# Kernel optimization log

Hardware: AMD Instinct MI355X
Metric: run time of the kernel (lower is better)

## Reference

```python
import jax, jax.numpy as jnp
import numpy as np

B, T, D_IN, H, K, C = 8, 2048, 512, 384, 8192, 8
N_BLOCKS = 6
EPS = 1e-5


def conv1d(x, w, b, pad, groups=1):
    # x: [B, Cin, T], w: [Cout, Cin//groups, k]
    y = jax.lax.conv_general_dilated(
        x, w, window_strides=(1,), padding=[(pad, pad)],
        dimension_numbers=("NCH", "OIH", "NCH"), feature_group_count=groups)
    return y + b[None, :, None]


def layernorm(x, g, b):
    # normalize over last axis
    m = jnp.mean(x, axis=-1, keepdims=True)
    v = jnp.mean(jnp.square(x - m), axis=-1, keepdims=True)
    return (x - m) * jax.lax.rsqrt(v + EPS) * g + b


def setup_inputs() -> dict:
    key = jax.random.key(0)
    ks = iter(jax.random.split(key, 32))
    s = 0.02
    inp = {
        "x": jax.random.normal(next(ks), (B, T, D_IN), dtype=jnp.float32),
        "enc_w": jax.random.normal(next(ks), (H, D_IN, 7)) * s,
        "enc_b": jnp.zeros((H,)),
        "enc_ln_g": jnp.ones((H,)),
        "enc_ln_b": jnp.zeros((H,)),
        "blk_dw_w": jax.random.normal(next(ks), (N_BLOCKS, H, 1, 7)) * s,
        "blk_dw_b": jnp.zeros((N_BLOCKS, H)),
        "blk_ln_g": jnp.ones((N_BLOCKS, H)),
        "blk_ln_b": jnp.zeros((N_BLOCKS, H)),
        "blk_w1": jax.random.normal(next(ks), (N_BLOCKS, 4 * H, H)) * s,
        "blk_b1": jnp.zeros((N_BLOCKS, 4 * H)),
        "blk_w2": jax.random.normal(next(ks), (N_BLOCKS, H, 4 * H)) * s,
        "blk_b2": jnp.zeros((N_BLOCKS, H)),
        "out_w": jax.random.normal(next(ks), (C, H, 1)) * s,
        "out_b": jnp.zeros((C,)),
        "embeddings": jax.random.normal(next(ks), (K, C)),
    }
    return inp


def encode(x, enc_w, enc_b, enc_ln_g, enc_ln_b, blk_dw_w, blk_dw_b,
           blk_ln_g, blk_ln_b, blk_w1, blk_b1, blk_w2, blk_b2, out_w, out_b):
    h = x.transpose(0, 2, 1)                       # [B, D_IN, T]
    h = conv1d(h, enc_w, enc_b, pad=3)             # [B, H, T]
    h = layernorm(h.transpose(0, 2, 1), enc_ln_g, enc_ln_b).transpose(0, 2, 1)
    for i in range(N_BLOCKS):
        res = h
        h = conv1d(h, blk_dw_w[i], blk_dw_b[i], pad=3, groups=H)  # depthwise
        ht = h.transpose(0, 2, 1)                  # [B, T, H]
        ht = layernorm(ht, blk_ln_g[i], blk_ln_b[i])
        ht = jnp.einsum("bth,fh->btf", ht, blk_w1[i]) + blk_b1[i]
        ht = jax.nn.gelu(ht, approximate=False)    # torch GELU is exact erf
        ht = jnp.einsum("btf,hf->bth", ht, blk_w2[i]) + blk_b2[i]
        h = ht.transpose(0, 2, 1) + res
    z = conv1d(h, out_w, out_b, pad=0)             # [B, C, T]
    return z.transpose(0, 2, 1)                    # [B, T, C]


def reference(x, enc_w, enc_b, enc_ln_g, enc_ln_b, blk_dw_w, blk_dw_b,
              blk_ln_g, blk_ln_b, blk_w1, blk_b1, blk_w2, blk_b2,
              out_w, out_b, embeddings):
    z = encode(x, enc_w, enc_b, enc_ln_g, enc_ln_b, blk_dw_w, blk_dw_b,
               blk_ln_g, blk_ln_b, blk_w1, blk_b1, blk_w2, blk_b2, out_w, out_b)
    flat = z.reshape(-1, C)                        # [B*T, C]
    # squared euclidean distances: same argmin as torch.cdist
    d2 = (jnp.sum(flat * flat, axis=1, keepdims=True)
          - 2.0 * flat @ embeddings.T
          + jnp.sum(embeddings * embeddings, axis=1))  # [B*T, K]
    indices = jnp.argmin(d2, axis=1)               # [B*T], int
    return indices
```

## Files before the change

### kernel.cpp

```cpp
#include <hip/hip_runtime.h>
#include <math.h>

#define T_   2048
#define DIN  512
#define H_   384
#define H4_  1536
#define BT_  16384

typedef _Float16 half_t;
typedef _Float16 f16x8 __attribute__((ext_vector_type(8)));
typedef float f32x4 __attribute__((ext_vector_type(4)));

#define LO_SCALE 2048.0f
#define LO_INV   4.8828125e-4f

__device__ __forceinline__ void lds_barrier() {
    asm volatile("s_waitcnt lgkmcnt(0)\n\ts_barrier" ::: "memory");
}

__device__ __forceinline__ void vm_barrier() {
    asm volatile("s_waitcnt vmcnt(0) lgkmcnt(0)\n\ts_barrier" ::: "memory");
}

__device__ __forceinline__ void gload_lds(const half_t* g, half_t* l) {
    __builtin_amdgcn_global_load_lds(
        (const __attribute__((address_space(1))) unsigned int*)(const void*)g,
        (__attribute__((address_space(3))) unsigned int*)(void*)l, 16, 0, 0);
}

__device__ __forceinline__ void split2(float v, half_t* hi, half_t* lo) {
    half_t h = (half_t)v;
    *hi = h;
    *lo = (half_t)((v - (float)h) * LO_SCALE);
}

__global__ void k_split(const float* __restrict__ in, half_t* __restrict__ hi,
                        half_t* __restrict__ lo, long n) {
    long i = (long)blockIdx.x * 256 + threadIdx.x;
    if (i >= n) return;
    split2(in[i], hi + i, lo + i);
}

__global__ void k_split_encw(const float* __restrict__ in, half_t* __restrict__ hi,
                             half_t* __restrict__ lo) {
    int idx = blockIdx.x * 256 + threadIdx.x;
    if (idx >= H_ * 3584) return;
    int n = idx / 3584;
    int r = idx % 3584;
    int tap = r >> 9, i = r & 511;
    split2(in[n * 3584 + i * 7 + tap], hi + idx, lo + idx);
}

__global__ void k_ln(const float* __restrict__ in, float* __restrict__ out,
                     const float* __restrict__ g, const float* __restrict__ b) {
    int row = blockIdx.x;
    int lane = threadIdx.x;
    const float* ir = in + (long)row * H_;
    float v[6];
    float s = 0.f;
#pragma unroll
    for (int j = 0; j < 6; ++j) { v[j] = ir[lane + (j << 6)]; s += v[j]; }
#pragma unroll
    for (int o = 32; o > 0; o >>= 1) s += __shfl_down(s, o, 64);
    s = __shfl(s, 0, 64);
    float mean = s * (1.f / 384.f);
    float q = 0.f;
#pragma unroll
    for (int j = 0; j < 6; ++j) { float d = v[j] - mean; q += d * d; }
#pragma unroll
    for (int o = 32; o > 0; o >>= 1) q += __shfl_down(q, o, 64);
    q = __shfl(q, 0, 64);
    float rstd = rsqrtf(q * (1.f / 384.f) + 1e-5f);
    float* orow = out + (long)row * H_;
#pragma unroll
    for (int j = 0; j < 6; ++j) {
        int c = lane + (j << 6);
        orow[c] = (v[j] - mean) * rstd * g[c] + b[c];
    }
}

__global__ __launch_bounds__(256) void k_dwconv_ln(
    const float* __restrict__ h, half_t* __restrict__ oh,
    half_t* __restrict__ ol,
    const float* __restrict__ w, const float* __restrict__ wb,
    const float* __restrict__ g, const float* __restrict__ gb) {
    int row = (blockIdx.x << 2) + (threadIdx.x >> 6);
    int b = row >> 11;
    int t = row & 2047;
    int lane = threadIdx.x & 63;
    const float* hb = h + ((long)b * T_) * H_;
    float vx[3], vy[3];
    float s = 0.f;
#pragma unroll
    for (int j = 0; j < 3; ++j) {
        int c = (lane << 1) + (j << 7);
        float ax = wb[c], ay = wb[c + 1];
        const float* wcx = w + c * 7;
        const float* wcy = wcx + 7;
#pragma unroll
        for (int k = 0; k < 7; ++k) {
            int tt = t + k - 3;
            if ((unsigned)tt < (unsigned)T_) {
                float2 hv = *(const float2*)&hb[(long)tt * H_ + c];
                ax = fmaf(hv.x, wcx[k], ax);
                ay = fmaf(hv.y, wcy[k], ay);
            }
        }
        vx[j] = ax; vy[j] = ay;
        s += ax + ay;
    }
#pragma unroll
    for (int o = 32; o > 0; o >>= 1) s += __shfl_down(s, o, 64);
    s = __shfl(s, 0, 64);
    float mean = s * (1.f / 384.f);
    float q = 0.f;
#pragma unroll
    for (int j = 0; j < 3; ++j) {
        float dx = vx[j] - mean, dy = vy[j] - mean;
        q += dx * dx + dy * dy;
    }
#pragma unroll
    for (int o = 32; o > 0; o >>= 1) q += __shfl_down(q, o, 64);
    q = __shfl(q, 0, 64);
    float rstd = rsqrtf(q * (1.f / 384.f) + 1e-5f);
    long ro = (long)row * H_;
#pragma unroll
    for (int j = 0; j < 3; ++j) {
        int c = (lane << 1) + (j << 7);
        float valx = (vx[j] - mean) * rstd * g[c] + gb[c];
        float valy = (vy[j] - mean) * rstd * g[c + 1] + gb[c + 1];
        split2(valx, oh + ro + c, ol + ro + c);
        split2(valy, oh + ro + c + 1, ol + ro + c + 1);
    }
}

#define DECLSET(S) float4 pAh##S, pAl##S, pBh0##S, pBl0##S, pBh1##S, pBl1##S

#define LOADREGS(S, k0_) do {                                               \
    int k0v = (k0_);                                                        \
    if (MODE == 0) {                                                        \
        int kk = k0v + ak;                                                  \
        int tap = kk >> 9, ii = kk & 511;                                   \
        int ta = tt0 + tap;                                                 \
        pAh##S = pAl##S = make_float4(0.f, 0.f, 0.f, 0.f);                  \
        if ((unsigned)ta < 2048u) {                                         \
            long o = ((long)bq * 2048 + ta) * 512 + ii;                     \
            pAh##S = *(const float4*)(Ah + o);                              \
            pAl##S = *(const float4*)(Al + o);                              \
        }                                                                   \
    } else {                                                                \
        pAh##S = *(const float4*)(Ah + aoff + k0v);                         \
        pAl##S = *(const float4*)(Al + aoff + k0v);                         \
    }                                                                       \
    pBh0##S = *(const float4*)(Bh + boff0 + k0v);                           \
    pBl0##S = *(const float4*)(Bl + boff0 + k0v);                           \
    pBh1##S = *(const float4*)(Bh + boff1 + k0v);                           \
    pBl1##S = *(const float4*)(Bl + boff1 + k0v);                           \
} while (0)

#define STOREBUF(S, buf) do {                                               \
    *(float4*)&smem[(buf) * 2048 + aw] = pAh##S;                            \
    *(float4*)&smem[4096 + (buf) * 2048 + aw] = pAl##S;                     \
    int b_ = 8192 + (buf) * 4096 + aw;                                      \
    *(float4*)&smem[b_] = pBh0##S;                                          \
    *(float4*)&smem[b_ + 2048] = pBh1##S;                                   \
    *(float4*)&smem[b_ + 8192] = pBl0##S;                                   \
    *(float4*)&smem[b_ + 8192 + 2048] = pBl1##S;                            \
} while (0)

template <int MODE, int NN>
__global__ __launch_bounds__(256, 3) void k_mgemm64(
    const half_t* __restrict__ Ah, const half_t* __restrict__ Al,
    const half_t* __restrict__ Bh, const half_t* __restrict__ Bl,
    const float* __restrict__ bias, const float* __restrict__ res,
    float* __restrict__ Cf, half_t* __restrict__ Ch, half_t* __restrict__ Cl,
    int N, int K) {
    __shared__ __align__(16) half_t smem[24576];
    const int tid = threadIdx.x;
    const int lane = tid & 63, wid = tid >> 6;
    const int wn = wid << 5;
    const int quad = lane >> 4, l16 = lane & 15;

    constexpr int NWG = 256 * NN;
    constexpr int CHUNK = NWG / 8;
    const int lin = blockIdx.x;
    const int tile = (lin & 7) * CHUNK + (lin >> 3);
    const int m0 = (tile / NN) << 6;
    const int n0 = (tile % NN) << 7;

    const int ar = tid >> 2;
    const int ak = (tid & 3) << 3;

    long aoff = 0;
    int tt0 = 0, bq = 0;
    if (MODE == 0) {
        bq = m0 >> 11;
        tt0 = (m0 & 2047) + ar - 3;
    } else {
        aoff = (long)(m0 + ar) * K + ak;
    }
    const long boff0 = (long)(n0 + ar) * K + ak;
    const long boff1 = boff0 + (long)64 * K;

    const int aw = ar * 32 + ((((tid & 3) ^ (ar >> 1)) & 3) << 3);

    DECLSET(0);
    DECLSET(1);

    f32x4 acc1[4][2] = {};
    f32x4 acc2[4][2] = {};
    const int sw = ((quad ^ (l16 >> 1)) & 3) << 3;

    auto compute = [&](int buf) {
        const int ab = buf * 2048 + l16 * 32 + sw;
        const int bb = 8192 + buf * 4096 + (wn + l16) * 32 + sw;
        f16x8 fah[4], fal[4], fgh[2], fgl[2];
#pragma unroll
        for (int f = 0; f < 4; ++f) {
            fah[f] = *(const f16x8*)&smem[ab + f * 512];
            fal[f] = *(const f16x8*)&smem[ab + 4096 + f * 512];
        }
#pragma unroll
        for (int g = 0; g < 2; ++g) {
            fgh[g] = *(const f16x8*)&smem[bb + g * 512];
            fgl[g] = *(const f16x8*)&smem[bb + 8192 + g * 512];
        }
#pragma unroll
        for (int f = 0; f < 4; ++f)
#pragma unroll
            for (int g = 0; g < 2; ++g)
                acc2[f][g] = __builtin_amdgcn_mfma_f32_16x16x32_f16(fah[f], fgl[g], acc2[f][g], 0, 0, 0);
#pragma unroll
        for (int f = 0; f < 4; ++f)
#pragma unroll
            for (int g = 0; g < 2; ++g)
                acc2[f][g] = __builtin_amdgcn_mfma_f32_16x16x32_f16(fal[f], fgh[g], acc2[f][g], 0, 0, 0);
#pragma unroll
        for (int f = 0; f < 4; ++f)
#pragma unroll
            for (int g = 0; g < 2; ++g)
                acc1[f][g] = __builtin_amdgcn_mfma_f32_16x16x32_f16(fah[f], fgh[g], acc1[f][g], 0, 0, 0);
    };

    const int nIter = K >> 5;
    LOADREGS(0, 0);
    LOADREGS(1, 32);
    STOREBUF(0, 0);
    if (nIter > 2) LOADREGS(0, 64);
    for (int it = 0; it < nIter; it += 2) {
        lds_barrier();
        compute(0);
        STOREBUF(1, 1);
        if (it + 3 < nIter) LOADREGS(1, (it + 3) << 5);
        lds_barrier();
        compute(1);
        if (it + 2 < nIter) {
            STOREBUF(0, 0);
            if (it + 4 < nIter) LOADREGS(0, (it + 4) << 5);
        }
    }

    float bv[2];
    bv[0] = bias[n0 + wn + l16];
    bv[1] = bias[n0 + wn + 16 + l16];

#pragma unroll
    for (int f = 0; f < 4; ++f)
#pragma unroll
        for (int g = 0; g < 2; ++g)
#pragma unroll
            for (int r = 0; r < 4; ++r) {
                long row = m0 + f * 16 + quad * 4 + r;
                int col = n0 + wn + g * 16 + l16;
                float v = acc1[f][g][r] + acc2[f][g][r] * LO_INV + bv[g];
                long o = row * N + col;
                if (MODE == 2) v += res[o];
                Cf[o] = v;
            }
}

template <int MODE, int NT>
__global__ __launch_bounds__(256, 2) void k_mgemm128(
    const half_t* __restrict__ Ah, const half_t* __restrict__ Al,
    const half_t* __restrict__ Bh, const half_t* __restrict__ Bl,
    const float* __restrict__ bias, const float* __restrict__ res,
    float* __restrict__ Cf, half_t* __restrict__ Ch, half_t* __restrict__ Cl,
    int N, int K) {
    __shared__ __align__(16) half_t smem[32768];
    const int tid = threadIdx.x;
    const int lane = tid & 63, wid = tid >> 6;
    const int wm = (wid >> 1) << 6;
    const int wn = (wid & 1) << 6;
    const int quad = lane >> 4, l16 = lane & 15;

    constexpr int NWG = 128 * NT;
    constexpr int CHUNK = NWG / 8;
    const int lin = blockIdx.x;
    const int tile = (lin & 7) * CHUNK + (lin >> 3);
    const int m0 = (tile / NT) << 7;
    const int n0 = (tile % NT) << 7;

    const int role = wid;
    const half_t* srcp = (role == 0) ? Ah : (role == 1) ? Al
                        : (role == 2) ? Bh : Bl;
    const int row0g = (role < 2) ? m0 : n0;
    const int lr = lane >> 2;
    const int lg = (lane & 3) ^ ((lane >> 3) & 3);
    const half_t* gbase = srcp + (long)(row0g + lr) * K + lg * 8;
    const long kstride = (long)16 * K;

#define STAGEDMA(buf, k0_) do {                                             \
    int k0v = (k0_);                                                        \
    _Pragma("unroll")                                                       \
    for (int i_ = 0; i_ < 8; ++i_)                                          \
        gload_lds(gbase + i_ * kstride + k0v,                               \
                  &smem[(buf) * 16384 + role * 4096 + i_ * 512]);           \
} while (0)

    f32x4 acc1[4][4] = {};
    f32x4 acc2[4][4] = {};
    const int sw = ((quad ^ (l16 >> 1)) & 3) << 3;

    auto compute = [&](int buf) {
        const int ab = buf * 16384 + (wm + l16) * 32 + sw;
        const int bb = buf * 16384 + 8192 + (wn + l16) * 32 + sw;
        f16x8 fah[4], fal[4], fgh[4], fgl[4];
#pragma unroll
        for (int f = 0; f < 4; ++f) {
            fah[f] = *(const f16x8*)&smem[ab + f * 512];
            fal[f] = *(const f16x8*)&smem[ab + 4096 + f * 512];
        }
#pragma unroll
        for (int g = 0; g < 4; ++g) {
            fgh[g] = *(const f16x8*)&smem[bb + g * 512];
            fgl[g] = *(const f16x8*)&smem[bb + 4096 + g * 512];
        }
#pragma unroll
        for (int f = 0; f < 4; ++f)
#pragma unroll
            for (int g = 0; g < 4; ++g)
                acc2[f][g] = __builtin_amdgcn_mfma_f32_16x16x32_f16(fah[f], fgl[g], acc2[f][g], 0, 0, 0);
#pragma unroll
        for (int f = 0; f < 4; ++f)
#pragma unroll
            for (int g = 0; g < 4; ++g)
                acc2[f][g] = __builtin_amdgcn_mfma_f32_16x16x32_f16(fal[f], fgh[g], acc2[f][g], 0, 0, 0);
#pragma unroll
        for (int f = 0; f < 4; ++f)
#pragma unroll
            for (int g = 0; g < 4; ++g)
                acc1[f][g] = __builtin_amdgcn_mfma_f32_16x16x32_f16(fah[f], fgh[g], acc1[f][g], 0, 0, 0);
    };

    const int nIter = K >> 5;
    STAGEDMA(0, 0);
    vm_barrier();
    int cur = 0;
    for (int it = 0; it < nIter; ++it) {
        if (it + 1 < nIter) STAGEDMA(cur ^ 1, (it + 1) << 5);
        compute(cur);
        vm_barrier();
        cur ^= 1;
    }
#undef STAGEDMA

    float bv[4];
#pragma unroll
    for (int g = 0; g < 4; ++g) bv[g] = bias[n0 + wn + g * 16 + l16];

    if (MODE == 1) {
#pragma unroll
        for (int p = 0; p < 2; ++p) {
            if ((wid >> 1) == p) {
#pragma unroll
                for (int f = 0; f < 4; ++f)
#pragma unroll
                    for (int g = 0; g < 4; ++g)
#pragma unroll
                        for (int r = 0; r < 4; ++r) {
                            int rm = f * 16 + quad * 4 + r;
                            int cn = wn + g * 16 + l16;
                            float v = acc1[f][g][r] + acc2[f][g][r] * LO_INV + bv[g];
                            v = 0.5f * v * (1.0f + erff(v * 0.70710678118654752f));
                            half_t hh = (half_t)v;
                            smem[rm * 136 + cn] = hh;
                            smem[8704 + rm * 136 + cn] = (half_t)((v - (float)hh) * LO_SCALE);
                        }
            }
            __syncthreads();
            int rrow = tid >> 2, c0 = (tid & 3) << 5;
            long go = (long)(m0 + p * 64 + rrow) * N + n0 + c0;
            int so = rrow * 136 + c0;
#pragma unroll
            for (int u = 0; u < 4; ++u) {
                *(float4*)(Ch + go + u * 8) = *(const float4*)&smem[so + u * 8];
                *(float4*)(Cl + go + u * 8) = *(const float4*)&smem[8704 + so + u * 8];
            }
            __syncthreads();
        }
    } else {
#pragma unroll
        for (int f = 0; f < 4; ++f)
#pragma unroll
            for (int g = 0; g < 4; ++g)
#pragma unroll
                for (int r = 0; r < 4; ++r) {
                    long row = m0 + wm + f * 16 + quad * 4 + r;
                    int col = n0 + wn + g * 16 + l16;
                    float v = acc1[f][g][r] + acc2[f][g][r] * LO_INV + bv[g];
                    long o = row * N + col;
                    v += res[o];
                    Cf[o] = v;
                }
    }
}

__global__ __launch_bounds__(256) void k_outconv_argmin(
    const float* __restrict__ h, const float* __restrict__ ow,
    const float* __restrict__ ob, const float* __restrict__ emb,
    int* __restrict__ outIdx) {
    __shared__ float hs[16][H_ + 1];
    __shared__ float zs[16][8];
    __shared__ float es[16 * 516];
    __shared__ float rb[16][16];
    __shared__ int ri[16][16];
    const int tid = threadIdx.x;
    const int row0 = blockIdx.x << 4;

    for (int i = tid; i < 16 * (H_ / 4); i += 256) {
        int r = i / 96;
        int c4 = (i % 96) << 2;
        float4 v = *(const float4*)&h[((long)(row0 + r)) * H_ + c4];
        hs[r][c4] = v.x; hs[r][c4 + 1] = v.y; hs[r][c4 + 2] = v.z; hs[r][c4 + 3] = v.w;
    }
    __syncthreads();

    if (tid < 128) {
        int r = tid & 15, c = tid >> 4;
        float acc = ob[c];
        const float* wc = ow + c * H_;
        for (int j = 0; j < H_; ++j) acc = fmaf(hs[r][j], wc[j], acc);
        zs[r][c] = acc;
    }
    __syncthreads();

    const int r = tid & 15;
    const int sl = tid >> 4;
    float z0 = zs[r][0], z1 = zs[r][1], z2 = zs[r][2], z3 = zs[r][3];
    float z4 = zs[r][4], z5 = zs[r][5], z6 = zs[r][6], z7 = zs[r][7];
    float best = 3.4e38f;
    int bi = 0;

    for (int ch = 0; ch < 8; ++ch) {
        __syncthreads();
        for (int i = tid; i < 2048; i += 256) {
            int e = i >> 1;
            int half = (i & 1) << 2;
            float4 src = *(const float4*)&emb[(((long)(ch << 10)) + e) * 8 + half];
            *(float4*)&es[(e >> 6) * 516 + ((e & 63) << 3) + half] = src;
        }
        __syncthreads();
        const float* ep = es + sl * 516;
        int gbase = (ch << 10) + (sl << 6);
#pragma unroll 4
        for (int j = 0; j < 64; ++j) {
            float4 e0 = *(const float4*)(ep + (j << 3));
            float4 e1 = *(const float4*)(ep + (j << 3) + 4);
            float t, d;
            t = e0.x - z0; d = t * t;
            t = e0.y - z1; d = fmaf(t, t, d);
            t = e0.z - z2; d = fmaf(t, t, d);
            t = e0.w - z3; d = fmaf(t, t, d);
            t = e1.x - z4; d = fmaf(t, t, d);
            t = e1.y - z5; d = fmaf(t, t, d);
            t = e1.z - z6; d = fmaf(t, t, d);
            t = e1.w - z7; d = fmaf(t, t, d);
            if (d < best) { best = d; bi = gbase + j; }
        }
    }
    rb[r][sl] = best;
    ri[r][sl] = bi;
    __syncthreads();
    if (sl == 0) {
        float bb = rb[r][0];
        int bbi = ri[r][0];
#pragma unroll
        for (int s2 = 1; s2 < 16; ++s2) {
            float v = rb[r][s2];
            int i2 = ri[r][s2];
            if (v < bb || (v == bb && i2 < bbi)) { bb = v; bbi = i2; }
        }
        outIdx[row0 + r] = bbi;
    }
}

extern "C" void kernel_launch(void* const* d_in, const int* in_sizes, int n_in,
                              void* d_out, int out_size, void* d_ws, size_t ws_size,
                              hipStream_t stream) {
    const float* x        = (const float*)d_in[0];
    const float* enc_w    = (const float*)d_in[1];
    const float* enc_b    = (const float*)d_in[2];
    const float* enc_ln_g = (const float*)d_in[3];
    const float* enc_ln_b = (const float*)d_in[4];
    const float* blk_dw_w = (const float*)d_in[5];
    const float* blk_dw_b = (const float*)d_in[6];
    const float* blk_ln_g = (const float*)d_in[7];
    const float* blk_ln_b = (const float*)d_in[8];
    const float* blk_w1   = (const float*)d_in[9];
    const float* blk_b1   = (const float*)d_in[10];
    const float* blk_w2   = (const float*)d_in[11];
    const float* blk_b2   = (const float*)d_in[12];
    const float* out_w    = (const float*)d_in[13];
    const float* out_b    = (const float*)d_in[14];
    const float* emb      = (const float*)d_in[15];
    int* out = (int*)d_out;

    char* base = (char*)d_ws;
    float*  h    = (float*)base;
    half_t* tmph = (half_t*)(base + 25165824);
    half_t* tmpl = (half_t*)(base + 37748736);
    half_t* ht4h = (half_t*)(base + 50331648);
    half_t* ht4l = (half_t*)(base + 100663296);
    half_t* ench = (half_t*)(base + 150994944);
    half_t* encl = (half_t*)(base + 153747456);
    half_t* w1h  = (half_t*)(base + 156499968);
    half_t* w1l  = (half_t*)(base + 163577856);
    half_t* w2h  = (half_t*)(base + 170655744);
    half_t* w2l  = (half_t*)(base + 177733632);
    half_t* xh = ht4h;
    half_t* xl = (half_t*)(base + 50331648 + 16777216);

    k_split<<<(8388608 + 255) / 256, 256, 0, stream>>>(x, xh, xl, 8388608L);
    k_split<<<(3538944 + 255) / 256, 256, 0, stream>>>(blk_w1, w1h, w1l, 3538944L);
    k_split<<<(3538944 + 255) / 256, 256, 0, stream>>>(blk_w2, w2h, w2l, 3538944L);
    k_split_encw<<<(H_ * 3584 + 255) / 256, 256, 0, stream>>>(enc_w, ench, encl);

    k_mgemm64<0, 3><<<768, 256, 0, stream>>>(xh, xl, ench, encl, enc_b,
                                             nullptr, h, nullptr, nullptr,
                                             H_, 3584);
    k_ln<<<BT_, 64, 0, stream>>>(h, h, enc_ln_g, enc_ln_b);

    for (int i = 0; i < 6; ++i) {
        k_dwconv_ln<<<BT_ / 4, 256, 0, stream>>>(h, tmph, tmpl, blk_dw_w + i * H_ * 7,
                                                 blk_dw_b + i * H_, blk_ln_g + i * H_,
                                                 blk_ln_b + i * H_);
        k_mgemm128<1, 12><<<1536, 256, 0, stream>>>(
            tmph, tmpl, w1h + (long)i * 589824, w1l + (long)i * 589824,
            blk_b1 + i * H4_, nullptr, nullptr, ht4h, ht4l, H4_, H_);
        k_mgemm128<2, 3><<<384, 256, 0, stream>>>(
            ht4h, ht4l, w2h + (long)i * 589824, w2l + (long)i * 589824,
            blk_b2 + i * H_, h, h, nullptr, nullptr, H_, H4_);
    }

    k_outconv_argmin<<<BT_ / 16, 256, 0, stream>>>(h, out_w, out_b, emb, out);
}
```

Baseline: 1.752 ms.

## Retile block GEMMs to 128x192 with 8 waves and triple-buffered LDS

Replaces the 128x128, 4-wave split-fp16 GEMM with a 128x192 tile run by 512 threads. Each wave computes a 64x48 sub-tile, and all waves share the global-to-LDS DMA work. The pipeline changes from double buffering with a full vmcnt(0) wait to triple buffering with partial vmcnt waits, so loads for step it+2 stay in flight while step it computes. The larger tile is meant to improve operand reuse and hide memory latency. In exchange it uses about 120KB of LDS per block, which limits occupancy, and it produces fewer blocks (1024 and 256 instead of 1536 and 384).

```diff
diff --git a/kernel.cpp b/kernel.cpp
--- a/kernel.cpp
+++ b/kernel.cpp
@@ -16,10 +16,6 @@
 
 __device__ __forceinline__ void lds_barrier() {
     asm volatile("s_waitcnt lgkmcnt(0)\n\ts_barrier" ::: "memory");
-}
-
-__device__ __forceinline__ void vm_barrier() {
-    asm volatile("s_waitcnt vmcnt(0) lgkmcnt(0)\n\ts_barrier" ::: "memory");
 }
 
 __device__ __forceinline__ void gload_lds(const half_t* g, half_t* l) {
@@ -280,17 +276,17 @@
 }
 
 template <int MODE, int NT>
-__global__ __launch_bounds__(256, 2) void k_mgemm128(
+__global__ __launch_bounds__(512, 2) void k_g192(
     const half_t* __restrict__ Ah, const half_t* __restrict__ Al,
     const half_t* __restrict__ Bh, const half_t* __restrict__ Bl,
     const float* __restrict__ bias, const float* __restrict__ res,
     float* __restrict__ Cf, half_t* __restrict__ Ch, half_t* __restrict__ Cl,
     int N, int K) {
-    __shared__ __align__(16) half_t smem[32768];
+    __shared__ __align__(16) half_t smem[61440];
     const int tid = threadIdx.x;
     const int lane = tid & 63, wid = tid >> 6;
-    const int wm = (wid >> 1) << 6;
-    const int wn = (wid & 1) << 6;
+    const int wm = (wid & 1) << 6;
+    const int wn = ((wid >> 1) & 3) * 48;
     const int quad = lane >> 4, l16 = lane & 15;
 
     constexpr int NWG = 128 * NT;
@@ -298,111 +294,122 @@
     const int lin = blockIdx.x;
     const int tile = (lin & 7) * CHUNK + (lin >> 3);
     const int m0 = (tile / NT) << 7;
-    const int n0 = (tile % NT) << 7;
-
-    const int role = wid;
-    const half_t* srcp = (role == 0) ? Ah : (role == 1) ? Al
-                        : (role == 2) ? Bh : Bl;
-    const int row0g = (role < 2) ? m0 : n0;
+    const int n0 = (tile % NT) * 192;
+
     const int lr = lane >> 2;
     const int lg = (lane & 3) ^ ((lane >> 3) & 3);
-    const half_t* gbase = srcp + (long)(row0g + lr) * K + lg * 8;
-    const long kstride = (long)16 * K;
-
-#define STAGEDMA(buf, k0_) do {                                             \
+    const half_t* gsrc[5];
+    int ldo[5];
+#pragma unroll
+    for (int j = 0; j < 5; ++j) {
+        int q = wid * 5 + j;
+        const half_t* sp;
+        long r0;
+        int lo_;
+        if (q < 8)       { sp = Ah; r0 = m0 + q * 16;        lo_ = q * 512; }
+        else if (q < 16) { sp = Al; r0 = m0 + (q - 8) * 16;  lo_ = 4096 + (q - 8) * 512; }
+        else if (q < 28) { sp = Bh; r0 = n0 + (q - 16) * 16; lo_ = 8192 + (q - 16) * 512; }
+        else             { sp = Bl; r0 = n0 + (q - 28) * 16; lo_ = 14336 + (q - 28) * 512; }
+        gsrc[j] = sp + (r0 + lr) * (long)K + lg * 8;
+        ldo[j] = lo_;
+    }
+
+#define STAGE3(bufb, k0_) do {                                              \
     int k0v = (k0_);                                                        \
     _Pragma("unroll")                                                       \
-    for (int i_ = 0; i_ < 8; ++i_)                                          \
-        gload_lds(gbase + i_ * kstride + k0v,                               \
-                  &smem[(buf) * 16384 + role * 4096 + i_ * 512]);           \
+    for (int j = 0; j < 5; ++j)                                             \
+        gload_lds(gsrc[j] + k0v, &smem[(bufb) + ldo[j]]);                   \
 } while (0)
 
-    f32x4 acc1[4][4] = {};
-    f32x4 acc2[4][4] = {};
+    f32x4 acc1[4][3] = {};
+    f32x4 acc2[4][3] = {};
     const int sw = ((quad ^ (l16 >> 1)) & 3) << 3;
 
-    auto compute = [&](int buf) {
-        const int ab = buf * 16384 + (wm + l16) * 32 + sw;
-        const int bb = buf * 16384 + 8192 + (wn + l16) * 32 + sw;
-        f16x8 fah[4], fal[4], fgh[4], fgl[4];
+    auto compute = [&](int bufb) {
+        const int ab = bufb + (wm + l16) * 32 + sw;
+        const int bb = bufb + 8192 + (wn + l16) * 32 + sw;
+        f16x8 fah[4], fal[4], fgh[3], fgl[3];
 #pragma unroll
         for (int f = 0; f < 4; ++f) {
             fah[f] = *(const f16x8*)&smem[ab + f * 512];
             fal[f] = *(const f16x8*)&smem[ab + 4096 + f * 512];
         }
 #pragma unroll
-        for (int g = 0; g < 4; ++g) {
+        for (int g = 0; g < 3; ++g) {
             fgh[g] = *(const f16x8*)&smem[bb + g * 512];
-            fgl[g] = *(const f16x8*)&smem[bb + 4096 + g * 512];
-        }
-#pragma unroll
-        for (int f = 0; f < 4; ++f)
-#pragma unroll
-            for (int g = 0; g < 4; ++g)
+            fgl[g] = *(const f16x8*)&smem[bb + 6144 + g * 512];
+        }
+#pragma unroll
+        for (int f = 0; f < 4; ++f)
+#pragma unroll
+            for (int g = 0; g < 3; ++g)
                 acc2[f][g] = __builtin_amdgcn_mfma_f32_16x16x32_f16(fah[f], fgl[g], acc2[f][g], 0, 0, 0);
 #pragma unroll
         for (int f = 0; f < 4; ++f)
 #pragma unroll
-            for (int g = 0; g < 4; ++g)
+            for (int g = 0; g < 3; ++g)
                 acc2[f][g] = __builtin_amdgcn_mfma_f32_16x16x32_f16(fal[f], fgh[g], acc2[f][g], 0, 0, 0);
 #pragma unroll
         for (int f = 0; f < 4; ++f)
 #pragma unroll
-            for (int g = 0; g < 4; ++g)
+            for (int g = 0; g < 3; ++g)
                 acc1[f][g] = __builtin_amdgcn_mfma_f32_16x16x32_f16(fah[f], fgh[g], acc1[f][g], 0, 0, 0);
     };
 
     const int nIter = K >> 5;
-    STAGEDMA(0, 0);
-    vm_barrier();
-    int cur = 0;
-    for (int it = 0; it < nIter; ++it) {
-        if (it + 1 < nIter) STAGEDMA(cur ^ 1, (it + 1) << 5);
-        compute(cur);
-        vm_barrier();
-        cur ^= 1;
-    }
-#undef STAGEDMA
-
-    float bv[4];
-#pragma unroll
-    for (int g = 0; g < 4; ++g) bv[g] = bias[n0 + wn + g * 16 + l16];
+    STAGE3(0, 0);
+    STAGE3(20480, 32);
+    int b0 = 0, b1 = 20480, b2 = 40960;
+    for (int it = 0; it + 2 < nIter; ++it) {
+        STAGE3(b2, (it + 2) << 5);
+        asm volatile("s_waitcnt vmcnt(10)" ::: "memory");
+        __builtin_amdgcn_s_barrier();
+        compute(b0);
+        __builtin_amdgcn_s_barrier();
+        int t_ = b0; b0 = b1; b1 = b2; b2 = t_;
+    }
+    asm volatile("s_waitcnt vmcnt(5)" ::: "memory");
+    __builtin_amdgcn_s_barrier();
+    compute(b0);
+    asm volatile("s_waitcnt vmcnt(0)" ::: "memory");
+    __builtin_amdgcn_s_barrier();
+    compute(b1);
+#undef STAGE3
+
+    float bv[3];
+#pragma unroll
+    for (int g = 0; g < 3; ++g) bv[g] = bias[n0 + wn + g * 16 + l16];
 
     if (MODE == 1) {
-#pragma unroll
-        for (int p = 0; p < 2; ++p) {
-            if ((wid >> 1) == p) {
-#pragma unroll
-                for (int f = 0; f < 4; ++f)
-#pragma unroll
-                    for (int g = 0; g < 4; ++g)
-#pragma unroll
-                        for (int r = 0; r < 4; ++r) {
-                            int rm = f * 16 + quad * 4 + r;
-                            int cn = wn + g * 16 + l16;
-                            float v = acc1[f][g][r] + acc2[f][g][r] * LO_INV + bv[g];
-                            v = 0.5f * v * (1.0f + erff(v * 0.70710678118654752f));
-                            half_t hh = (half_t)v;
-                            smem[rm * 136 + cn] = hh;
-                            smem[8704 + rm * 136 + cn] = (half_t)((v - (float)hh) * LO_SCALE);
-                        }
-            }
-            __syncthreads();
-            int rrow = tid >> 2, c0 = (tid & 3) << 5;
-            long go = (long)(m0 + p * 64 + rrow) * N + n0 + c0;
-            int so = rrow * 136 + c0;
-#pragma unroll
-            for (int u = 0; u < 4; ++u) {
-                *(float4*)(Ch + go + u * 8) = *(const float4*)&smem[so + u * 8];
-                *(float4*)(Cl + go + u * 8) = *(const float4*)&smem[8704 + so + u * 8];
-            }
-            __syncthreads();
+        __syncthreads();
+#pragma unroll
+        for (int f = 0; f < 4; ++f)
+#pragma unroll
+            for (int g = 0; g < 3; ++g)
+#pragma unroll
+                for (int r = 0; r < 4; ++r) {
+                    int rm = wm + f * 16 + quad * 4 + r;
+                    int cn = wn + g * 16 + l16;
+                    float v = acc1[f][g][r] + acc2[f][g][r] * LO_INV + bv[g];
+                    v = 0.5f * v * (1.0f + erff(v * 0.70710678118654752f));
+                    half_t hh = (half_t)v;
+                    smem[rm * 200 + cn] = hh;
+                    smem[25600 + rm * 200 + cn] = (half_t)((v - (float)hh) * LO_SCALE);
+                }
+        __syncthreads();
+        int row = tid >> 2, c0 = (tid & 3) * 48;
+        long go = (long)(m0 + row) * N + n0 + c0;
+        int so = row * 200 + c0;
+#pragma unroll
+        for (int u = 0; u < 6; ++u) {
+            *(float4*)(Ch + go + u * 8) = *(const float4*)&smem[so + u * 8];
+            *(float4*)(Cl + go + u * 8) = *(const float4*)&smem[25600 + so + u * 8];
         }
     } else {
 #pragma unroll
         for (int f = 0; f < 4; ++f)
 #pragma unroll
-            for (int g = 0; g < 4; ++g)
+            for (int g = 0; g < 3; ++g)
 #pragma unroll
                 for (int r = 0; r < 4; ++r) {
                     long row = m0 + wm + f * 16 + quad * 4 + r;
@@ -544,10 +551,10 @@
         k_dwconv_ln<<<BT_ / 4, 256, 0, stream>>>(h, tmph, tmpl, blk_dw_w + i * H_ * 7,
                                                  blk_dw_b + i * H_, blk_ln_g + i * H_,
                                                  blk_ln_b + i * H_);
-        k_mgemm128<1, 12><<<1536, 256, 0, stream>>>(
+        k_g192<1, 8><<<1024, 512, 0, stream>>>(
             tmph, tmpl, w1h + (long)i * 589824, w1l + (long)i * 589824,
             blk_b1 + i * H4_, nullptr, nullptr, ht4h, ht4l, H4_, H_);
-        k_mgemm128<2, 3><<<384, 256, 0, stream>>>(
+        k_g192<2, 2><<<256, 512, 0, stream>>>(
             ht4h, ht4l, w2h + (long)i * 589824, w2l + (long)i * 589824,
             blk_b2 + i * H_, h, h, nullptr, nullptr, H_, H4_);
     }
```

After: 1.733 ms. Within noise of the previous version (-1.1%).
